# Optimization experiments

Measured on AMD Instinct MI355X. Metric: run time of the kernel, lower is better.

## Reference

```python
import jax, jax.numpy as jnp
import numpy as np

N, K, IN_C, OUT_C, EDGE_D = 50000, 32, 128, 64, 32
E = N * K
MSG_EPS = 1e-7
BN_EPS = 1e-5


def setup_inputs() -> dict:
    rng = np.random.default_rng(0)
    # Consistent graph: edge e has destination e // K; nbr[n] lists n's edges, -1-padded.
    nbr = np.arange(E, dtype=np.int64).reshape(N, K)
    deg = rng.integers(K // 2, K + 1, size=N)
    nbr = np.where(np.arange(K)[None, :] < deg[:, None], nbr, -1)
    dst = np.repeat(np.arange(N, dtype=np.int64), K)
    src = rng.integers(0, N, size=E).astype(np.int64)
    edge_index = np.stack([src, dst])

    key = jax.random.key(0)
    ks = jax.random.split(key, 8)
    init = lambda k, shape, fan: (jax.random.normal(k, shape, jnp.float32) / np.sqrt(fan)).astype(jnp.float32)
    return {
        "x": jax.random.normal(ks[0], (N, IN_C), jnp.float32),
        "edge_attr": jax.random.normal(ks[1], (E, EDGE_D), jnp.float32),
        "w_src": init(ks[2], (OUT_C, IN_C), IN_C),
        "w_dst": init(ks[3], (OUT_C, IN_C), IN_C),
        "w_edge": init(ks[4], (OUT_C, EDGE_D), EDGE_D),
        "w1": init(ks[5], (2 * OUT_C, OUT_C), OUT_C),
        "gamma": jnp.ones((2 * OUT_C,), jnp.float32),
        "beta": jnp.zeros((2 * OUT_C,), jnp.float32),
        "w2": init(ks[6], (OUT_C, 2 * OUT_C), 2 * OUT_C),
        "edge_index": jnp.asarray(edge_index),
        "nbr": jnp.asarray(nbr),
    }


def _gather_sum(src, nbr_idx, valid):
    # src: [E,H] per-edge values; nbr_idx: [N,K] clamped edge ids; valid: [N,K]
    g = src[nbr_idx]                                   # [N,K,H]
    return jnp.where(valid[..., None], g, 0.0).sum(axis=1)  # [N,H]


def reference(x, edge_attr, w_src, w_dst, w_edge, w1, gamma, beta, w2, edge_index, nbr):
    valid = nbr >= 0
    nidx = jnp.clip(nbr, 0)
    src_n, dest = edge_index[0], edge_index[1]

    src = x @ w_src.T                                  # [N,H]
    dst_feat = x @ w_dst.T                             # [N,H]
    x_j = src[src_n]                                   # [E,H]
    msg = jax.nn.relu(x_j + edge_attr @ w_edge.T) + MSG_EPS  # [E,H]

    # softmax over each destination's neighbor edges (gather-max / gather-sum via nbr)
    neg = -jnp.finfo(msg.dtype).max
    gmax = jnp.where(valid[..., None], msg[nidx], neg).max(axis=1)   # [N,H]
    alpha = jnp.exp(msg - gmax[dest])                                # [E,H]
    denom = _gather_sum(alpha, nidx, valid) + 1e-16                  # [N,H]
    alpha = alpha / denom[dest]

    out = _gather_sum(msg * alpha, nidx, valid) + dst_feat           # [N,H]

    # MLP: Linear -> BatchNorm1d(train-mode batch stats, biased var) -> ReLU -> Linear
    h = out @ w1.T                                     # [N,2H]
    mean = h.mean(axis=0)
    var = h.var(axis=0)
    h = (h - mean) * jax.lax.rsqrt(var + BN_EPS) * gamma + beta
    h = jax.nn.relu(h)
    return h @ w2.T                                    # [N,H]
```

## Files before the change

### kernel.cpp

```cpp
#include <hip/hip_runtime.h>
#include <hip/hip_bf16.h>
#include <float.h>

#define NN 50000
#define KNB 32
#define INC 128
#define HC 64
#define EDD 32
#define H2C 128
#define NBLK 782

typedef __attribute__((ext_vector_type(8))) short bf16x8;
typedef __attribute__((ext_vector_type(4))) float f32x4;
typedef __attribute__((ext_vector_type(4))) _Float16 f16x4;

__device__ __forceinline__ short f2bf(float f) {
    unsigned u = __builtin_bit_cast(unsigned, f);
    u += 0x7fffu + ((u >> 16) & 1u);
    return (short)(u >> 16);
}
__device__ __forceinline__ float bf2f(short h) {
    unsigned u = ((unsigned)(unsigned short)h) << 16;
    return __builtin_bit_cast(float, u);
}

__device__ __forceinline__ bf16x8 pack8_bf16(const float* av) {
    union { unsigned u[4]; bf16x8 v; } r;
    #pragma unroll
    for (int w = 0; w < 4; ++w) {
        asm("v_cvt_pk_bf16_f32 %0, %1, %2"
            : "=v"(r.u[w]) : "v"(av[2 * w]), "v"(av[2 * w + 1]));
    }
    return r.v;
}

__global__ __launch_bounds__(256) void k_prep(
    const float* __restrict__ w_src, const float* __restrict__ w_dst,
    const float* __restrict__ w1, const float* __restrict__ w2,
    const float* __restrict__ w_edge,
    short* __restrict__ pAhi, short* __restrict__ pAlo,
    short* __restrict__ p1hi, short* __restrict__ p1lo,
    short* __restrict__ p2hi, short* __restrict__ p2lo,
    short* __restrict__ pE)
{
    const int tid = blockIdx.x * 256 + threadIdx.x;
    const int nT  = gridDim.x * 256;
    for (int idx = tid; idx < 16384; idx += nT) {
        int kt = (idx >> 12) & 3, nt = (idx >> 9) & 7, lane = (idx >> 3) & 63, j = idx & 7;
        int lr = lane & 15, lg = lane >> 4;
        int ch = nt * 16 + lr, k = kt * 32 + lg * 8 + j;
        float f = (ch < 64) ? w_src[ch * 128 + k] : w_dst[(ch - 64) * 128 + k];
        short hi = f2bf(f);
        pAhi[idx] = hi; pAlo[idx] = f2bf(f - bf2f(hi));
    }
    for (int idx = tid; idx < 8192; idx += nT) {
        int kt = (idx >> 12) & 1, nt = (idx >> 9) & 7, lane = (idx >> 3) & 63, j = idx & 7;
        int lr = lane & 15, lg = lane >> 4;
        int ch = nt * 16 + lr, k = kt * 32 + lg * 8 + j;
        float f = w1[ch * 64 + k];
        short hi = f2bf(f);
        p1hi[idx] = hi; p1lo[idx] = f2bf(f - bf2f(hi));
    }
    for (int idx = tid; idx < 8192; idx += nT) {
        int kt = (idx >> 11) & 3, nt = (idx >> 9) & 3, lane = (idx >> 3) & 63, j = idx & 7;
        int lr = lane & 15, lg = lane >> 4;
        int ch = nt * 16 + lr, k = kt * 32 + lg * 8 + j;
        float f = w2[ch * 128 + k];
        short hi = f2bf(f);
        p2hi[idx] = hi; p2lo[idx] = f2bf(f - bf2f(hi));
    }
    for (int idx = tid; idx < 2048; idx += nT) {
        int nt = (idx >> 9) & 3, lane = (idx >> 3) & 63, j = idx & 7;
        int lr = lane & 15, lg = lane >> 4;
        int ch = nt * 16 + lr, k = lg * 8 + j;
        pE[idx] = f2bf(w_edge[ch * EDD + k]);
    }
}

__device__ __forceinline__ void split8(const float* av, bf16x8& ahi, bf16x8& alo) {
    #pragma unroll
    for (int j = 0; j < 8; ++j) {
        short h = f2bf(av[j]);
        ahi[j] = h;
        alo[j] = f2bf(av[j] - bf2f(h));
    }
}

__global__ __launch_bounds__(256) void k_lin1(
    const float* __restrict__ x, const short* __restrict__ pAhi,
    const short* __restrict__ pAlo, _Float16* __restrict__ srcPh,
    float* __restrict__ dstf)
{
    const int lane = threadIdx.x & 63, wave = threadIdx.x >> 6;
    const int lr = lane & 15, lg = lane >> 4;
    const int nb = blockIdx.x * 64 + wave * 16;
    const bf16x8* Bh = (const bf16x8*)pAhi;
    const bf16x8* Bl = (const bf16x8*)pAlo;
    int row = nb + lr; if (row > NN - 1) row = NN - 1;

    f32x4 acc[8];
    #pragma unroll
    for (int i = 0; i < 8; ++i) acc[i] = (f32x4){0.f, 0.f, 0.f, 0.f};

    #pragma unroll
    for (int kt = 0; kt < 4; ++kt) {
        const float* ap = x + (size_t)row * INC + kt * 32 + lg * 8;
        float4 a0 = *(const float4*)ap, a1 = *(const float4*)(ap + 4);
        float av[8] = {a0.x, a0.y, a0.z, a0.w, a1.x, a1.y, a1.z, a1.w};
        bf16x8 ahi, alo;
        split8(av, ahi, alo);
        #pragma unroll
        for (int nt = 0; nt < 8; ++nt) {
            bf16x8 bh = Bh[(kt * 8 + nt) * 64 + lane];
            bf16x8 bl = Bl[(kt * 8 + nt) * 64 + lane];
            acc[nt] = __builtin_amdgcn_mfma_f32_16x16x32_bf16(ahi, bl, acc[nt], 0, 0, 0);
            acc[nt] = __builtin_amdgcn_mfma_f32_16x16x32_bf16(alo, bh, acc[nt], 0, 0, 0);
            acc[nt] = __builtin_amdgcn_mfma_f32_16x16x32_bf16(ahi, bh, acc[nt], 0, 0, 0);
        }
    }
    #pragma unroll
    for (int nt = 0; nt < 8; ++nt)
        #pragma unroll
        for (int q = 0; q < 4; ++q) {
            int node = nb + lg * 4 + q;
            if (node < NN) {
                float v = acc[nt][q];
                if (nt < 4) srcPh[node * HC + lr * 4 + nt] = (_Float16)v;
                else        dstf[node * HC + (nt - 4) * 16 + lr] = v;
            }
        }
}

__global__ __launch_bounds__(256) void k_edge_agg_mfma(
    const _Float16* __restrict__ srcPh, const float* __restrict__ dstf,
    const float* __restrict__ edge_attr, const short* __restrict__ pE,
    const int* __restrict__ esrc, const int* __restrict__ nbr,
    float* __restrict__ outf)
{
    const int lane = threadIdx.x & 63;
    const int wave = threadIdx.x >> 6;
    const int n    = blockIdx.x * 4 + wave;
    const int lr = lane & 15, lg = lane >> 4;

    int4 s0 = *(const int4*)&esrc[n * KNB + lg * 4];
    int4 s1 = *(const int4*)&esrc[n * KNB + 16 + lg * 4];
    int nbv   = nbr[n * KNB + (lane & 31)];
    float d   = dstf[n * HC + lane];

    const bf16x8* Bp = (const bf16x8*)pE;
    bf16x8 bfrag[4];
    #pragma unroll
    for (int nt = 0; nt < 4; ++nt) bfrag[nt] = Bp[nt * 64 + lane];

    const f32x4* ab = (const f32x4*)(edge_attr + (size_t)n * KNB * EDD);
    f32x4 at[4];
    #pragma unroll
    for (int mt = 0; mt < 2; ++mt) {
        int off = ((mt * 16 + lr) * EDD + lg * 8) >> 2;
        at[mt * 2]     = __builtin_nontemporal_load(ab + off);
        at[mt * 2 + 1] = __builtin_nontemporal_load(ab + off + 1);
    }

    int i0[4] = {s0.x, s0.y, s0.z, s0.w};
    int i1[4] = {s1.x, s1.y, s1.z, s1.w};
    f16x4 xj0[4], xj1[4];
    #pragma unroll
    for (int r = 0; r < 4; ++r)
        xj0[r] = *(const f16x4*)(srcPh + (((unsigned)i0[r] << 6) + lr * 4));
    #pragma unroll
    for (int r = 0; r < 4; ++r)
        xj1[r] = *(const f16x4*)(srcPh + (((unsigned)i1[r] << 6) + lr * 4));

    unsigned vmask = (unsigned)__ballot((lane < 32) && (nbv >= 0));

    bf16x8 afrag[2];
    #pragma unroll
    for (int mt = 0; mt < 2; ++mt) {
        float av[8] = {at[mt*2][0], at[mt*2][1], at[mt*2][2], at[mt*2][3],
                       at[mt*2+1][0], at[mt*2+1][1], at[mt*2+1][2], at[mt*2+1][3]};
        afrag[mt] = pack8_bf16(av);
    }

    f32x4 p[2][4];
    #pragma unroll
    for (int mt = 0; mt < 2; ++mt)
        #pragma unroll
        for (int nt = 0; nt < 4; ++nt) {
            f32x4 z = {0.f, 0.f, 0.f, 0.f};
            p[mt][nt] = __builtin_amdgcn_mfma_f32_16x16x32_bf16(
                afrag[mt], bfrag[nt], z, 0, 0, 0);
        }

    float vf[4];
    #pragma unroll
    for (int r = 0; r < 4; ++r)
        vf[r] = ((vmask >> (16 + lg * 4 + r)) & 1u) ? 1.f : 0.f;

    float res[4];
    #pragma unroll
    for (int nt = 0; nt < 4; ++nt) {
        float se = 0.f, ws = 0.f;
        #pragma unroll
        for (int r = 0; r < 4; ++r) {
            float m = fmaxf(p[0][nt][r] + (float)xj0[r][nt], 0.f);
            float t = __expf(m);
            se += t;
            ws = fmaf(m, t, ws);
        }
        #pragma unroll
        for (int r = 0; r < 4; ++r) {
            float m = fmaxf(p[1][nt][r] + (float)xj1[r][nt], 0.f);
            float t = __expf(m) * vf[r];
            se += t;
            ws = fmaf(m, t, ws);
        }
        se += __shfl_xor(se, 16, 64); ws += __shfl_xor(ws, 16, 64);
        se += __shfl_xor(se, 32, 64); ws += __shfl_xor(ws, 32, 64);
        res[nt] = ws * __builtin_amdgcn_rcpf(se + 1e-16f);
    }

    float r01 = (lg & 1) ? res[1] : res[0];
    float r23 = (lg & 1) ? res[3] : res[2];
    float rr  = (lg & 2) ? r23 : r01;
    outf[n * HC + lane] = rr + d + 1e-7f;
}

__global__ __launch_bounds__(256) void k_lin2(
    const float* __restrict__ outf, const short* __restrict__ p1hi,
    const short* __restrict__ p1lo, float* __restrict__ h,
    float* __restrict__ partials)
{
    __shared__ float ps[128 * 16], pq[128 * 16];
    const int t = threadIdx.x;
    const int lane = t & 63, wave = t >> 6;
    const int lr = lane & 15, lg = lane >> 4;
    const int nb = blockIdx.x * 64 + wave * 16;
    const bf16x8* Bh = (const bf16x8*)p1hi;
    const bf16x8* Bl = (const bf16x8*)p1lo;
    int row = nb + lr; if (row > NN - 1) row = NN - 1;

    f32x4 acc[8];
    #pragma unroll
    for (int i = 0; i < 8; ++i) acc[i] = (f32x4){0.f, 0.f, 0.f, 0.f};

    #pragma unroll
    for (int kt = 0; kt < 2; ++kt) {
        const float* ap = outf + (size_t)row * HC + kt * 32 + lg * 8;
        float4 a0 = *(const float4*)ap, a1 = *(const float4*)(ap + 4);
        float av[8] = {a0.x, a0.y, a0.z, a0.w, a1.x, a1.y, a1.z, a1.w};
        bf16x8 ahi, alo;
        split8(av, ahi, alo);
        #pragma unroll
        for (int nt = 0; nt < 8; ++nt) {
            bf16x8 bh = Bh[(kt * 8 + nt) * 64 + lane];
            bf16x8 bl = Bl[(kt * 8 + nt) * 64 + lane];
            acc[nt] = __builtin_amdgcn_mfma_f32_16x16x32_bf16(ahi, bl, acc[nt], 0, 0, 0);
            acc[nt] = __builtin_amdgcn_mfma_f32_16x16x32_bf16(alo, bh, acc[nt], 0, 0, 0);
            acc[nt] = __builtin_amdgcn_mfma_f32_16x16x32_bf16(ahi, bh, acc[nt], 0, 0, 0);
        }
    }

    #pragma unroll
    for (int nt = 0; nt < 8; ++nt) {
        float s = 0.f, q = 0.f;
        #pragma unroll
        for (int qq = 0; qq < 4; ++qq) {
            int node = nb + lg * 4 + qq;
            float v = acc[nt][qq];
            if (node < NN) {
                h[node * H2C + nt * 16 + lr] = v;
                s += v;
                q += v * v;
            }
        }
        ps[(nt * 16 + lr) * 16 + wave * 4 + lg] = s;
        pq[(nt * 16 + lr) * 16 + wave * 4 + lg] = q;
    }
    __syncthreads();
    if (t < 128) {
        float s = 0.f, q = 0.f;
        #pragma unroll
        for (int i = 0; i < 16; ++i) { s += ps[t * 16 + i]; q += pq[t * 16 + i]; }
        partials[blockIdx.x * 256 + t]       = s;
        partials[blockIdx.x * 256 + 128 + t] = q;
    }
}

__global__ __launch_bounds__(1024) void k_bn_finalize(
    const float* __restrict__ partials, int nblk,
    const float* __restrict__ gamma, const float* __restrict__ beta,
    float* __restrict__ sb)
{
    const int t = threadIdx.x;
    const int f = t & 63;
    const int g = t >> 6;

    float4 acc = {0.f, 0.f, 0.f, 0.f};
    for (int b = g; b < nblk; b += 16) {
        float4 v = *(const float4*)&partials[b * 256 + f * 4];
        acc.x += v.x; acc.y += v.y; acc.z += v.z; acc.w += v.w;
    }

    __shared__ __align__(16) float4 red[16][64];
    red[g][f] = acc;
    __syncthreads();
    #pragma unroll
    for (int s = 8; s > 0; s >>= 1) {
        if (g < s) {
            float4 o = red[g + s][f];
            acc.x += o.x; acc.y += o.y; acc.z += o.z; acc.w += o.w;
            red[g][f] = acc;
        }
        __syncthreads();
    }

    if (t < 128) {
        const float* row = (const float*)&red[0][0];
        float s = row[t];
        float q = row[128 + t];
        float mean = s / (float)NN;
        float var  = q / (float)NN - mean * mean;
        float scale = gamma[t] * rsqrtf(var + 1e-5f);
        float bias  = beta[t] - mean * scale;
        sb[t]       = scale;
        sb[128 + t] = bias;
    }
}

__global__ __launch_bounds__(256) void k_lin3(
    const float* __restrict__ h, const short* __restrict__ p2hi,
    const short* __restrict__ p2lo, const float* __restrict__ sb,
    float* __restrict__ out)
{
    const int lane = threadIdx.x & 63, wave = threadIdx.x >> 6;
    const int lr = lane & 15, lg = lane >> 4;
    const int nb = blockIdx.x * 64 + wave * 16;
    const bf16x8* Bh = (const bf16x8*)p2hi;
    const bf16x8* Bl = (const bf16x8*)p2lo;
    int row = nb + lr; if (row > NN - 1) row = NN - 1;

    f32x4 acc[4];
    #pragma unroll
    for (int i = 0; i < 4; ++i) acc[i] = (f32x4){0.f, 0.f, 0.f, 0.f};

    #pragma unroll
    for (int kt = 0; kt < 4; ++kt) {
        const int k0 = kt * 32 + lg * 8;
        float4 sc0 = *(const float4*)&sb[k0],       sc1 = *(const float4*)&sb[k0 + 4];
        float4 bi0 = *(const float4*)&sb[128 + k0], bi1 = *(const float4*)&sb[128 + k0 + 4];
        const float* ap = h + (size_t)row * H2C + k0;
        float4 a0 = *(const float4*)ap, a1 = *(const float4*)(ap + 4);
        float av[8]  = {a0.x, a0.y, a0.z, a0.w, a1.x, a1.y, a1.z, a1.w};
        float scv[8] = {sc0.x, sc0.y, sc0.z, sc0.w, sc1.x, sc1.y, sc1.z, sc1.w};
        float biv[8] = {bi0.x, bi0.y, bi0.z, bi0.w, bi1.x, bi1.y, bi1.z, bi1.w};
        float rv[8];
        #pragma unroll
        for (int j = 0; j < 8; ++j) {
            float v = av[j] * scv[j] + biv[j];
            rv[j] = v > 0.f ? v : 0.f;
        }
        bf16x8 ahi, alo;
        split8(rv, ahi, alo);
        #pragma unroll
        for (int nt = 0; nt < 4; ++nt) {
            bf16x8 bh = Bh[(kt * 4 + nt) * 64 + lane];
            bf16x8 bl = Bl[(kt * 4 + nt) * 64 + lane];
            acc[nt] = __builtin_amdgcn_mfma_f32_16x16x32_bf16(ahi, bl, acc[nt], 0, 0, 0);
            acc[nt] = __builtin_amdgcn_mfma_f32_16x16x32_bf16(alo, bh, acc[nt], 0, 0, 0);
            acc[nt] = __builtin_amdgcn_mfma_f32_16x16x32_bf16(ahi, bh, acc[nt], 0, 0, 0);
        }
    }
    #pragma unroll
    for (int nt = 0; nt < 4; ++nt)
        #pragma unroll
        for (int q = 0; q < 4; ++q) {
            int node = nb + lg * 4 + q;
            if (node < NN) out[node * HC + nt * 16 + lr] = acc[nt][q];
        }
}

extern "C" void kernel_launch(void* const* d_in, const int* in_sizes, int n_in,
                              void* d_out, int out_size, void* d_ws, size_t ws_size,
                              hipStream_t stream) {
    const float* x         = (const float*)d_in[0];
    const float* edge_attr = (const float*)d_in[1];
    const float* w_src     = (const float*)d_in[2];
    const float* w_dst     = (const float*)d_in[3];
    const float* w_edge    = (const float*)d_in[4];
    const float* w1        = (const float*)d_in[5];
    const float* gamma     = (const float*)d_in[6];
    const float* beta      = (const float*)d_in[7];
    const float* w2        = (const float*)d_in[8];
    const int*   eidx      = (const int*)d_in[9];
    const int*   nbr       = (const int*)d_in[10];

    float* ws   = (float*)d_ws;
    _Float16* srcPh = (_Float16*)ws;
    float* dstf = ws + 3200000;
    float* outf = ws + 6400000;
    float* h    = ws + 9600000;
    float* part = ws + 16000000;
    float* sb   = ws + 16250000;
    short* sp   = (short*)(ws + 16300000);
    short* pAhi = sp;
    short* pAlo = sp + 16384;
    short* p1hi = sp + 32768;
    short* p1lo = sp + 40960;
    short* p2hi = sp + 49152;
    short* p2lo = sp + 57344;
    short* pE   = sp + 65536;

    hipLaunchKernelGGL(k_prep,          dim3(32),    dim3(256),  0, stream,
                       w_src, w_dst, w1, w2, w_edge,
                       pAhi, pAlo, p1hi, p1lo, p2hi, p2lo, pE);
    hipLaunchKernelGGL(k_lin1,          dim3(NBLK),  dim3(256),  0, stream,
                       x, pAhi, pAlo, srcPh, dstf);
    hipLaunchKernelGGL(k_edge_agg_mfma, dim3(12500), dim3(256),  0, stream,
                       srcPh, dstf, edge_attr, pE, eidx, nbr, outf);
    hipLaunchKernelGGL(k_lin2,          dim3(NBLK),  dim3(256),  0, stream,
                       outf, p1hi, p1lo, h, part);
    hipLaunchKernelGGL(k_bn_finalize,   dim3(1),     dim3(1024), 0, stream,
                       part, NBLK, gamma, beta, sb);
    hipLaunchKernelGGL(k_lin3,          dim3(NBLK),  dim3(256),  0, stream,
                       h, p2hi, p2lo, sb, (float*)d_out);
}
```

Baseline: 131.5 us.

## Split each node's edge aggregation across two waves with LDS reduction

The edge-aggregation kernel now assigns two waves per destination node, each handling one 16-edge half (one MFMA M-tile), instead of one wave per node handling both halves. Partial softmax sums and weighted sums are combined through shared memory after a block barrier, and the grid doubles to 25000 blocks. The aim is more memory-level parallelism and shorter per-wave dependency chains for the gather-heavy step. The cost is more waves, duplicated B-fragment loads, LDS traffic, a __syncthreads, and half the waves idling at the final store.

Measured after the change: 134.7 us. 2.5% more time.

```diff
diff --git a/kernel.cpp b/kernel.cpp
--- a/kernel.cpp
+++ b/kernel.cpp
@@ -137,92 +137,86 @@
     const int* __restrict__ esrc, const int* __restrict__ nbr,
     float* __restrict__ outf)
 {
+    __shared__ float sered[2][2][64];
+    __shared__ float wsred[2][2][64];
+
     const int lane = threadIdx.x & 63;
     const int wave = threadIdx.x >> 6;
-    const int n    = blockIdx.x * 4 + wave;
+    const int nl   = wave >> 1;
+    const int mt   = wave & 1;
+    const int node = blockIdx.x * 2 + nl;
     const int lr = lane & 15, lg = lane >> 4;
 
-    int4 s0 = *(const int4*)&esrc[n * KNB + lg * 4];
-    int4 s1 = *(const int4*)&esrc[n * KNB + 16 + lg * 4];
-    int nbv   = nbr[n * KNB + (lane & 31)];
-    float d   = dstf[n * HC + lane];
+    int4 sv = *(const int4*)&esrc[node * KNB + mt * 16 + lg * 4];
+
+    int nbv = nbr[node * KNB + 16 + (lane & 15)];
+    float d = (mt == 0) ? dstf[node * HC + lane] : 0.f;
 
     const bf16x8* Bp = (const bf16x8*)pE;
     bf16x8 bfrag[4];
     #pragma unroll
     for (int nt = 0; nt < 4; ++nt) bfrag[nt] = Bp[nt * 64 + lane];
 
-    const f32x4* ab = (const f32x4*)(edge_attr + (size_t)n * KNB * EDD);
-    f32x4 at[4];
-    #pragma unroll
-    for (int mt = 0; mt < 2; ++mt) {
-        int off = ((mt * 16 + lr) * EDD + lg * 8) >> 2;
-        at[mt * 2]     = __builtin_nontemporal_load(ab + off);
-        at[mt * 2 + 1] = __builtin_nontemporal_load(ab + off + 1);
-    }
-
-    int i0[4] = {s0.x, s0.y, s0.z, s0.w};
-    int i1[4] = {s1.x, s1.y, s1.z, s1.w};
-    f16x4 xj0[4], xj1[4];
+    const f32x4* ab = (const f32x4*)(edge_attr + (size_t)node * KNB * EDD);
+    int aoff = ((mt * 16 + lr) * EDD + lg * 8) >> 2;
+    f32x4 at0 = __builtin_nontemporal_load(ab + aoff);
+    f32x4 at1 = __builtin_nontemporal_load(ab + aoff + 1);
+
+    int iv[4] = {sv.x, sv.y, sv.z, sv.w};
+    f16x4 xj[4];
     #pragma unroll
     for (int r = 0; r < 4; ++r)
-        xj0[r] = *(const f16x4*)(srcPh + (((unsigned)i0[r] << 6) + lr * 4));
+        xj[r] = *(const f16x4*)(srcPh + (((unsigned)iv[r] << 6) + lr * 4));
+
+    unsigned vmask = (unsigned)__ballot((lane < 16) && (nbv >= 0));
+
+    float av[8] = {at0[0], at0[1], at0[2], at0[3], at1[0], at1[1], at1[2], at1[3]};
+    bf16x8 afrag = pack8_bf16(av);
+
+    f32x4 p[4];
+    #pragma unroll
+    for (int nt = 0; nt < 4; ++nt) {
+        f32x4 z = {0.f, 0.f, 0.f, 0.f};
+        p[nt] = __builtin_amdgcn_mfma_f32_16x16x32_bf16(afrag, bfrag[nt], z, 0, 0, 0);
+    }
+
+    float vf[4];
     #pragma unroll
     for (int r = 0; r < 4; ++r)
-        xj1[r] = *(const f16x4*)(srcPh + (((unsigned)i1[r] << 6) + lr * 4));
-
-    unsigned vmask = (unsigned)__ballot((lane < 32) && (nbv >= 0));
-
-    bf16x8 afrag[2];
-    #pragma unroll
-    for (int mt = 0; mt < 2; ++mt) {
-        float av[8] = {at[mt*2][0], at[mt*2][1], at[mt*2][2], at[mt*2][3],
-                       at[mt*2+1][0], at[mt*2+1][1], at[mt*2+1][2], at[mt*2+1][3]};
-        afrag[mt] = pack8_bf16(av);
-    }
-
-    f32x4 p[2][4];
-    #pragma unroll
-    for (int mt = 0; mt < 2; ++mt)
-        #pragma unroll
-        for (int nt = 0; nt < 4; ++nt) {
-            f32x4 z = {0.f, 0.f, 0.f, 0.f};
-            p[mt][nt] = __builtin_amdgcn_mfma_f32_16x16x32_bf16(
-                afrag[mt], bfrag[nt], z, 0, 0, 0);
-        }
-
-    float vf[4];
-    #pragma unroll
-    for (int r = 0; r < 4; ++r)
-        vf[r] = ((vmask >> (16 + lg * 4 + r)) & 1u) ? 1.f : 0.f;
-
-    float res[4];
+        vf[r] = (mt == 0) ? 1.f : (((vmask >> (lg * 4 + r)) & 1u) ? 1.f : 0.f);
+
+    float se[4], ws[4];
     #pragma unroll
     for (int nt = 0; nt < 4; ++nt) {
-        float se = 0.f, ws = 0.f;
+        float s = 0.f, w = 0.f;
         #pragma unroll
         for (int r = 0; r < 4; ++r) {
-            float m = fmaxf(p[0][nt][r] + (float)xj0[r][nt], 0.f);
-            float t = __expf(m);
-            se += t;
-            ws = fmaf(m, t, ws);
-        }
-        #pragma unroll
-        for (int r = 0; r < 4; ++r) {
-            float m = fmaxf(p[1][nt][r] + (float)xj1[r][nt], 0.f);
+            float m = fmaxf(p[nt][r] + (float)xj[r][nt], 0.f);
             float t = __expf(m) * vf[r];
-            se += t;
-            ws = fmaf(m, t, ws);
-        }
-        se += __shfl_xor(se, 16, 64); ws += __shfl_xor(ws, 16, 64);
-        se += __shfl_xor(se, 32, 64); ws += __shfl_xor(ws, 32, 64);
-        res[nt] = ws * __builtin_amdgcn_rcpf(se + 1e-16f);
-    }
-
-    float r01 = (lg & 1) ? res[1] : res[0];
-    float r23 = (lg & 1) ? res[3] : res[2];
-    float rr  = (lg & 2) ? r23 : r01;
-    outf[n * HC + lane] = rr + d + 1e-7f;
+            s += t;
+            w = fmaf(m, t, w);
+        }
+        s += __shfl_xor(s, 16, 64); w += __shfl_xor(w, 16, 64);
+        s += __shfl_xor(s, 32, 64); w += __shfl_xor(w, 32, 64);
+        se[nt] = s; ws[nt] = w;
+    }
+
+    float s01 = (lg & 1) ? se[1] : se[0];
+    float s23 = (lg & 1) ? se[3] : se[2];
+    float ssel = (lg & 2) ? s23 : s01;
+    float w01 = (lg & 1) ? ws[1] : ws[0];
+    float w23 = (lg & 1) ? ws[3] : ws[2];
+    float wsel = (lg & 2) ? w23 : w01;
+    sered[nl][mt][lane] = ssel;
+    wsred[nl][mt][lane] = wsel;
+    __syncthreads();
+
+    if (mt == 0) {
+        float seT = sered[nl][0][lane] + sered[nl][1][lane];
+        float wsT = wsred[nl][0][lane] + wsred[nl][1][lane];
+        float res = wsT * __builtin_amdgcn_rcpf(seT + 1e-16f);
+        outf[node * HC + lane] = res + d + 1e-7f;
+    }
 }
 
 __global__ __launch_bounds__(256) void k_lin2(
@@ -415,7 +409,7 @@
                        pAhi, pAlo, p1hi, p1lo, p2hi, p2lo, pE);
     hipLaunchKernelGGL(k_lin1,          dim3(NBLK),  dim3(256),  0, stream,
                        x, pAhi, pAlo, srcPh, dstf);
-    hipLaunchKernelGGL(k_edge_agg_mfma, dim3(12500), dim3(256),  0, stream,
+    hipLaunchKernelGGL(k_edge_agg_mfma, dim3(25000), dim3(256),  0, stream,
                        srcPh, dstf, edge_attr, pE, eidx, nbr, outf);
     hipLaunchKernelGGL(k_lin2,          dim3(NBLK),  dim3(256),  0, stream,
                        outf, p1hi, p1lo, h, part);
```
